# Performance work log

Hardware: AMD Instinct MI355X
Metric: run time of the kernel (lower is better)

The kernel has to match this reference:

```python
import jax, jax.numpy as jnp
import numpy as np

EMBED_DIM = 1024
NUM_HEADS = 16
HEAD_DIM = EMBED_DIM // NUM_HEADS


def setup_inputs() -> dict:
    key = jax.random.key(0)
    ks = jax.random.split(key, 5)
    s = 0.02
    return {
        "x": jax.random.normal(ks[0], (2, 2048, EMBED_DIM), dtype=jnp.float32),
        "w_qkv": jax.random.normal(ks[1], (EMBED_DIM, 3 * EMBED_DIM), dtype=jnp.float32) * s,
        "b_qkv": jnp.zeros((3 * EMBED_DIM,), dtype=jnp.float32),
        "w_out": jax.random.normal(ks[2], (EMBED_DIM, EMBED_DIM), dtype=jnp.float32) * s,
        "b_out": jnp.zeros((EMBED_DIM,), dtype=jnp.float32),
    }


def reference(x, w_qkv, b_qkv, w_out, b_out):
    B, T, C = x.shape
    qkv = x @ w_qkv + b_qkv                       # [B,T,3C]
    q, k, v = jnp.split(qkv, 3, axis=-1)
    # [B,T,C] -> [B,H,T,Dh]
    def heads(t):
        return t.reshape(B, T, NUM_HEADS, HEAD_DIM).transpose(0, 2, 1, 3)
    q, k, v = heads(q), heads(k), heads(v)
    scale = 1.0 / np.sqrt(HEAD_DIM).astype(np.float32)
    scores = jnp.einsum("bhqd,bhkd->bhqk", q, k) * scale  # [B,H,T,T]
    causal = jnp.tril(jnp.ones((T, T), dtype=bool))
    scores = jnp.where(causal[None, None], scores, -jnp.inf)
    attn = jax.nn.softmax(scores, axis=-1)
    out = jnp.einsum("bhqk,bhkd->bhqd", attn, v)  # [B,H,T,Dh]
    out = out.transpose(0, 2, 1, 3).reshape(B, T, C)
    return out @ w_out + b_out
```

## Files before the change

kernel.cpp:

```cpp
#include <hip/hip_runtime.h>

typedef unsigned short u16;
typedef unsigned int u32;
typedef __attribute__((ext_vector_type(2))) unsigned int u32x2;
typedef __attribute__((ext_vector_type(8))) short bf16x8;
typedef __attribute__((ext_vector_type(4))) float f32x4;
typedef __attribute__((ext_vector_type(16))) float f32x16;

#define TOK   4096
#define EMB   1024
#define NQKV  3072
#define TSEQ  2048
#define NH    16

__device__ __forceinline__ u16 f2b(float f) {
  union { float f; unsigned u; } v; v.f = f;
  unsigned r = v.u + 0x7FFFu + ((v.u >> 16) & 1u);
  return (u16)(r >> 16);
}

__device__ __forceinline__ u16 f2b_hu(float f) {
  return (u16)((__float_as_uint(f) + 0x8000u) >> 16);
}

__device__ __forceinline__ u32 pack_rn(float a, float b) {
  u32 ua = __float_as_uint(a) + 0x8000u;
  u32 ub = __float_as_uint(b) + 0x8000u;
  return __builtin_amdgcn_perm(ub, ua, 0x07060302u);
}

__device__ __forceinline__ f32x16 zero16() {
  f32x16 z;
#pragma unroll
  for (int i = 0; i < 16; i++) z[i] = 0.f;
  return z;
}

__device__ __forceinline__ void gload16(const void* g, void* l) {
  __builtin_amdgcn_global_load_lds((const __attribute__((address_space(1))) void*)g,
                                   (__attribute__((address_space(3))) void*)l, 16, 0, 0);
}


__global__ __launch_bounds__(256) void prep_kernel(const float* __restrict__ x,
                                                   u16* __restrict__ x_bf,
                                                   const float* __restrict__ w_qkv,
                                                   u16* __restrict__ wqkvT,
                                                   const float* __restrict__ w_out,
                                                   u16* __restrict__ woutT) {
  __shared__ u16 sm[64][65];
  int bid = blockIdx.x, tid = threadIdx.x;
  if (bid < 4096) {
    int i = bid * 256 + tid;
    float4 v = ((const float4*)x)[i];
    union { u16 us[4]; uint2 u2; } o;
    o.us[0] = f2b(v.x); o.us[1] = f2b(v.y); o.us[2] = f2b(v.z); o.us[3] = f2b(v.w);
    ((uint2*)x_bf)[i] = o.u2;
    return;
  }
  const float* src; u16* dst; int R, C, bx, by;
  if (bid < 4096 + 768) {
    int t = bid - 4096; bx = t % 48; by = t / 48;
    src = w_qkv; dst = wqkvT; R = EMB; C = NQKV;
  } else {
    int t = bid - 4096 - 768; bx = t & 15; by = t >> 4;
    src = w_out; dst = woutT; R = EMB; C = EMB;
  }
  int c0 = bx * 64, r0 = by * 64;
#pragma unroll
  for (int i = 0; i < 16; i++) {
    int idx = tid + i * 256;
    int r = idx >> 6, c = idx & 63;
    sm[r][c] = f2b(src[(size_t)(r0 + r) * C + c0 + c]);
  }
  __syncthreads();
  int cc2 = tid >> 2, rr0 = (tid & 3) * 16;
  union { u16 us[16]; uint4 v4[2]; } o;
#pragma unroll
  for (int j = 0; j < 16; j++) o.us[j] = sm[rr0 + j][cc2];
  *(uint4*)&dst[(size_t)(c0 + cc2) * R + r0 + rr0]     = o.v4[0];
  *(uint4*)&dst[(size_t)(c0 + cc2) * R + r0 + rr0 + 8] = o.v4[1];
}


template <int MODE, int TN>
__global__ __launch_bounds__(256) void gemm_bt(const u16* __restrict__ A,
                                               const u16* __restrict__ Bt,
                                               const float* __restrict__ bias,
                                               u16* __restrict__ qb, u16* __restrict__ kb,
                                               u16* __restrict__ vb, float* __restrict__ outp,
                                               int K, int N) {
  constexpr int CT = TN / 32;
  constexpr int RB = TN / 32;
  __shared__ u16 As[2][128][64];
  __shared__ u16 Bs[2][TN][64];
  int tid = threadIdx.x;
  int m0 = blockIdx.y * 128, n0 = blockIdx.x * TN;
  int lane = tid & 63, wid = tid >> 6;
  int wm = (wid >> 1) * 64;
  int wn = (wid & 1) * (TN / 2);
  int l15 = lane & 15, quad = lane >> 4;
  int srow = lane >> 3;
  int scol = (((lane & 7) ^ srow) * 8);

  f32x4 acc[4][CT];
#pragma unroll
  for (int i = 0; i < 4; i++)
#pragma unroll
    for (int j = 0; j < CT; j++) acc[i][j] = (f32x4){0.f, 0.f, 0.f, 0.f};

  const u16* Ag = A + (size_t)(m0 + wid * 32 + srow) * K + scol;
  const u16* Bg = Bt + (size_t)(n0 + wid * (TN / 4) + srow) * K + scol;

#pragma unroll
  for (int i = 0; i < 4; i++)
    gload16(Ag + (size_t)(i * 8) * K, &As[0][wid * 32 + i * 8][0]);
#pragma unroll
  for (int i = 0; i < RB; i++)
    gload16(Bg + (size_t)(i * 8) * K, &Bs[0][wid * (TN / 4) + i * 8][0]);
  __syncthreads();

  int cur = 0;
  for (int k0 = 0; k0 < K; k0 += 64) {
    if (k0 + 64 < K) {
      int kn = k0 + 64;
#pragma unroll
      for (int i = 0; i < 4; i++)
        gload16(Ag + (size_t)(i * 8) * K + kn, &As[cur ^ 1][wid * 32 + i * 8][0]);
#pragma unroll
      for (int i = 0; i < RB; i++)
        gload16(Bg + (size_t)(i * 8) * K + kn, &Bs[cur ^ 1][wid * (TN / 4) + i * 8][0]);
    }

#pragma unroll
    for (int ks = 0; ks < 2; ks++) {
      bf16x8 af[4], bfr[CT];
#pragma unroll
      for (int rt = 0; rt < 4; rt++)
        af[rt] = *(const bf16x8*)&As[cur][wm + rt * 16 + l15][((ks * 4 + quad) ^ (l15 & 7)) * 8];
#pragma unroll
      for (int ct = 0; ct < CT; ct++)
        bfr[ct] = *(const bf16x8*)&Bs[cur][wn + ct * 16 + l15][((ks * 4 + quad) ^ (l15 & 7)) * 8];
#pragma unroll
      for (int rt = 0; rt < 4; rt++)
#pragma unroll
        for (int ct = 0; ct < CT; ct++)
          acc[rt][ct] = __builtin_amdgcn_mfma_f32_16x16x32_bf16(bfr[ct], af[rt], acc[rt][ct], 0, 0, 0);
    }
    __syncthreads();
    cur ^= 1;
  }

#pragma unroll
  for (int rt = 0; rt < 4; rt++) {
#pragma unroll
    for (int ct = 0; ct < CT; ct++) {
      int m = m0 + wm + rt * 16 + l15;
      int nb = n0 + wn + ct * 16 + quad * 4;
      float4 b4 = *(const float4*)&bias[nb];
      float v0 = acc[rt][ct][0] + b4.x, v1 = acc[rt][ct][1] + b4.y;
      float v2 = acc[rt][ct][2] + b4.z, v3 = acc[rt][ct][3] + b4.w;
      if (MODE == 0) {
        int sel = nb >> 10;
        int c = nb & 1023;
        int h = c >> 6, d0 = c & 63;
        int b = m >> 11, t = m & 2047;
        if (sel == 2) {
          size_t vbase = ((((size_t)b * NH + h) * 64 + d0) * TSEQ) + t;
          vb[vbase]            = f2b_hu(v0);
          vb[vbase + TSEQ]     = f2b_hu(v1);
          vb[vbase + 2 * TSEQ] = f2b_hu(v2);
          vb[vbase + 3 * TSEQ] = f2b_hu(v3);
        } else {
          u16* dst = sel ? kb : qb;
          union { u32 u[2]; uint2 u2; } o;
          o.u[0] = pack_rn(v0, v1);
          o.u[1] = pack_rn(v2, v3);
          *(uint2*)&dst[((((size_t)b * NH + h) * TSEQ + t) << 6) + d0] = o.u2;
        }
      } else {
        float4 o = {v0, v1, v2, v3};
        *(float4*)&outp[(size_t)m * N + nb] = o;
      }
    }
  }
}


__global__ __launch_bounds__(256, 4) void attn_kernel(const u16* __restrict__ Qb,
                                                      const u16* __restrict__ Kb,
                                                      const u16* __restrict__ Vtb,
                                                      u16* __restrict__ O) {
  __shared__ u16 Ks[64][68];
  __shared__ u16 Vt[64][68];
  __shared__ float Cmb[2][16][64][2];
  __shared__ float Lmb[2][32];

  const float SCL = 0.18033688f;
  const float MOFF = 16.0f;

  int phys = blockIdx.x;
  int xcd = phys & 7;
  int cuL = (phys >> 3) & 31;
  int slot = phys >> 8;
  int bh = xcd * 4 + slot;
  int qt = (slot & 1) ? (31 - cuL) : cuL;

  int tid = threadIdx.x, lane = tid & 63, w = tid >> 6;
  int sub = w & 1, par = w >> 1;
  int l31 = lane & 31, h = lane >> 5;
  const size_t hoff = (size_t)bh * TSEQ * 64;

  int qw = qt * 64 + sub * 32;
  int qg = qw + l31;

  bf16x8 qf[4];
  {
    const u16* qp = Qb + hoff + (size_t)qg * 64 + h * 8;
#pragma unroll
    for (int s = 0; s < 4; s++) qf[s] = *(const bf16x8*)(qp + s * 16);
  }

  f32x16 acc[2];
  acc[0] = zero16(); acc[1] = zero16();
  float l_i = 0.f;

  int r = tid >> 2, cb = (tid & 3) * 16;
  bf16x8 kr0, kr1, vr0, vr1;
  {
    const u16* kg = Kb + hoff + (size_t)r * 64 + cb;
    const u16* vg = Vtb + hoff + (size_t)r * TSEQ + cb;
    kr0 = *(const bf16x8*)kg;       kr1 = *(const bf16x8*)(kg + 8);
    vr0 = *(const bf16x8*)vg;       vr1 = *(const bf16x8*)(vg + 8);
  }

  for (int kt = 0; kt <= qt; kt++) {
    __syncthreads();
    *(bf16x8*)&Ks[r][cb]     = kr0;
    *(bf16x8*)&Ks[r][cb + 8] = kr1;
    *(bf16x8*)&Vt[r][cb]     = vr0;
    *(bf16x8*)&Vt[r][cb + 8] = vr1;
    __syncthreads();
    if (kt < qt) {
      const u16* kg = Kb + hoff + (size_t)((kt + 1) * 64 + r) * 64 + cb;
      const u16* vg = Vtb + hoff + (size_t)r * TSEQ + (kt + 1) * 64 + cb;
      kr0 = *(const bf16x8*)kg;     kr1 = *(const bf16x8*)(kg + 8);
      vr0 = *(const bf16x8*)vg;     vr1 = *(const bf16x8*)(vg + 8);
    }

    int kbt = kt * 64 + par * 32;
    if (kbt <= qw + 31) {
      f32x16 sacc = zero16();
      __builtin_amdgcn_s_setprio(1);
#pragma unroll
      for (int s = 0; s < 4; s++) {
        bf16x8 kf = *(const bf16x8*)&Ks[par * 32 + l31][s * 16 + h * 8];
        sacc = __builtin_amdgcn_mfma_f32_32x32x16_bf16(kf, qf[s], sacc, 0, 0, 0);
      }
      __builtin_amdgcn_s_setprio(0);

      if (kbt + 31 > qw) {
#pragma unroll
        for (int rr = 0; rr < 16; rr++) {
          int key = kbt + (rr & 3) + 8 * (rr >> 2) + 4 * h;
          if (key > qg) sacc[rr] = -1e30f;
        }
      }

#pragma unroll
      for (int rr = 0; rr < 16; rr++) {
        float p = exp2f(__builtin_fmaf(sacc[rr], SCL, -MOFF));
        sacc[rr] = p;
        l_i += p;
      }

#pragma unroll
      for (int s2 = 0; s2 < 2; s2++) {
        u32 u0, u1, u2, u3;
        asm("v_cvt_pk_bf16_f32 %0, %1, %2" : "=v"(u0) : "v"(sacc[8 * s2 + 0]), "v"(sacc[8 * s2 + 1]));
        asm("v_cvt_pk_bf16_f32 %0, %1, %2" : "=v"(u1) : "v"(sacc[8 * s2 + 2]), "v"(sacc[8 * s2 + 3]));
        asm("v_cvt_pk_bf16_f32 %0, %1, %2" : "=v"(u2) : "v"(sacc[8 * s2 + 4]), "v"(sacc[8 * s2 + 5]));
        asm("v_cvt_pk_bf16_f32 %0, %1, %2" : "=v"(u3) : "v"(sacc[8 * s2 + 6]), "v"(sacc[8 * s2 + 7]));
        u32x2 r02 = __builtin_amdgcn_permlane32_swap(u0, u2, false, false);
        u32x2 r13 = __builtin_amdgcn_permlane32_swap(u1, u3, false, false);
        union { u32 d[4]; bf16x8 v; } pf;
        pf.d[0] = r02[0];
        pf.d[1] = r13[0];
        pf.d[2] = r02[1];
        pf.d[3] = r13[1];
        __builtin_amdgcn_s_setprio(1);
#pragma unroll
        for (int dt = 0; dt < 2; dt++) {
          bf16x8 vf = *(const bf16x8*)&Vt[dt * 32 + l31][par * 32 + s2 * 16 + h * 8];
          acc[dt] = __builtin_amdgcn_mfma_f32_32x32x16_bf16(vf, pf.v, acc[dt], 0, 0, 0);
        }
        __builtin_amdgcn_s_setprio(0);
      }
    }
  }

  l_i += __shfl_xor(l_i, 32);

  __syncthreads();
  if (par == 1) {
#pragma unroll
    for (int dt = 0; dt < 2; dt++)
#pragma unroll
      for (int pr = 0; pr < 8; pr++) {
        Cmb[sub][dt * 8 + pr][lane][0] = acc[dt][2 * pr];
        Cmb[sub][dt * 8 + pr][lane][1] = acc[dt][2 * pr + 1];
      }
    if (h == 0) Lmb[sub][l31] = l_i;
  }
  __syncthreads();
  if (par == 0) {
#pragma unroll
    for (int dt = 0; dt < 2; dt++)
#pragma unroll
      for (int pr = 0; pr < 8; pr++) {
        acc[dt][2 * pr]     += Cmb[sub][dt * 8 + pr][lane][0];
        acc[dt][2 * pr + 1] += Cmb[sub][dt * 8 + pr][lane][1];
      }
    float lt = l_i + Lmb[sub][l31];
    float inv = 1.0f / lt;

    int b = bh >> 4, head = bh & 15;
    size_t rowbase = ((size_t)b * TSEQ + qg) * 1024 + head * 64;
#pragma unroll
    for (int dt = 0; dt < 2; dt++)
#pragma unroll
      for (int G = 0; G < 4; G++) {
        union { u32 u[2]; uint2 u2; } o;
        o.u[0] = pack_rn(acc[dt][4 * G + 0] * inv, acc[dt][4 * G + 1] * inv);
        o.u[1] = pack_rn(acc[dt][4 * G + 2] * inv, acc[dt][4 * G + 3] * inv);
        *(uint2*)&O[rowbase + dt * 32 + G * 8 + 4 * h] = o.u2;
      }
  }
}


extern "C" void kernel_launch(void* const* d_in, const int* in_sizes, int n_in,
                              void* d_out, int out_size, void* d_ws, size_t ws_size,
                              hipStream_t stream) {
  (void)in_sizes; (void)n_in; (void)out_size; (void)ws_size;
  const float* x     = (const float*)d_in[0];
  const float* w_qkv = (const float*)d_in[1];
  const float* b_qkv = (const float*)d_in[2];
  const float* w_out = (const float*)d_in[3];
  const float* b_out = (const float*)d_in[4];
  float* out = (float*)d_out;

  char* p = (char*)d_ws;
  u16* x_bf  = (u16*)p; p += (size_t)TOK * EMB * 2;
  u16* wqkvT = (u16*)p; p += (size_t)NQKV * EMB * 2;
  u16* woutT = (u16*)p; p += (size_t)EMB * EMB * 2;
  u16* Qb    = (u16*)p; p += (size_t)32 * TSEQ * 64 * 2;
  u16* Kb    = (u16*)p; p += (size_t)32 * TSEQ * 64 * 2;
  u16* Vtb   = (u16*)p; p += (size_t)32 * TSEQ * 64 * 2;
  u16* attn_o = (u16*)p;

  prep_kernel<<<dim3(4096 + 768 + 256), 256, 0, stream>>>(x, x_bf, w_qkv, wqkvT, w_out, woutT);
  gemm_bt<0, 128><<<dim3(NQKV / 128, TOK / 128), 256, 0, stream>>>(x_bf, wqkvT, b_qkv,
                                                                   Qb, Kb, Vtb, nullptr, EMB, NQKV);
  attn_kernel<<<dim3(1024), 256, 0, stream>>>(Qb, Kb, Vtb, attn_o);
  gemm_bt<1, 64><<<dim3(EMB / 64, TOK / 128), 256, 0, stream>>>(attn_o, woutT, b_out,
                                                                nullptr, nullptr, nullptr, out, EMB, EMB);
}
```

Measured before the change: 181.4 us.

## Add dedicated 256x192-tile QKV GEMM with 512 threads and interleaved prefetch

Replaces the generic 128x128 gemm_bt for the QKV projection with a specialized kernel using 256x192 tiles, 8 waves, and launch_bounds(512,1). Global-to-LDS prefetch of the next K step is split into phases interleaved with MFMA groups, with s_barrier and setprio around compute. The larger tile raises arithmetic intensity per LDS byte, and the grid becomes 16x16=256 blocks, roughly one per CU. The cost is heavier register and LDS use, and a single wave of blocks leaves no slack for load imbalance.

```diff
diff --git a/kernel.cpp b/kernel.cpp
--- a/kernel.cpp
+++ b/kernel.cpp
@@ -80,6 +80,119 @@
   for (int j = 0; j < 16; j++) o.us[j] = sm[rr0 + j][cc2];
   *(uint4*)&dst[(size_t)(c0 + cc2) * R + r0 + rr0]     = o.v4[0];
   *(uint4*)&dst[(size_t)(c0 + cc2) * R + r0 + rr0 + 8] = o.v4[1];
+}
+
+
+__global__ __launch_bounds__(512, 1) void gemm_qkv(const u16* __restrict__ A,
+                                                   const u16* __restrict__ Bt,
+                                                   const float* __restrict__ bias,
+                                                   u16* __restrict__ qb, u16* __restrict__ kb,
+                                                   u16* __restrict__ vb) {
+  constexpr int K = EMB;
+  constexpr int NSTEP = K / 64;
+  __shared__ u16 As[2][256][64];
+  __shared__ u16 Bs[2][192][64];
+  int tid = threadIdx.x;
+  int m0 = blockIdx.y * 256, n0 = blockIdx.x * 192;
+  int lane = tid & 63, wid = tid >> 6;
+  int wm = (wid >> 2) * 128;
+  int wn = (wid & 3) * 48;
+  int l15 = lane & 15, quad = lane >> 4;
+  int srow = lane >> 3;
+  int scol = ((lane & 7) ^ srow) * 8;
+
+  f32x4 acc[8][3];
+#pragma unroll
+  for (int i = 0; i < 8; i++)
+#pragma unroll
+    for (int j = 0; j < 3; j++) acc[i][j] = (f32x4){0.f, 0.f, 0.f, 0.f};
+
+  const u16* Ag = A + (size_t)(m0 + wid * 32 + srow) * K + scol;
+  const u16* Bg = Bt + (size_t)(n0 + wid * 24 + srow) * K + scol;
+
+#pragma unroll
+  for (int i = 0; i < 4; i++)
+    gload16(Ag + (size_t)(i * 8) * K, &As[0][wid * 32 + i * 8][0]);
+#pragma unroll
+  for (int i = 0; i < 3; i++)
+    gload16(Bg + (size_t)(i * 8) * K, &Bs[0][wid * 24 + i * 8][0]);
+  __syncthreads();
+
+  for (int t = 0; t < NSTEP; t++) {
+    int cur = t & 1;
+    int kn = (t + 1) * 64;
+    bool pf = (t + 1 < NSTEP);
+    bf16x8 bfr[3];
+#pragma unroll
+    for (int ks = 0; ks < 2; ks++) {
+#pragma unroll
+      for (int rh = 0; rh < 2; rh++) {
+        const int ph = ks * 2 + rh;
+        if (pf) {
+          if (ph == 0) {
+            gload16(Ag + (size_t)0 * K + kn,  &As[cur ^ 1][wid * 32 + 0][0]);
+            gload16(Ag + (size_t)8 * K + kn,  &As[cur ^ 1][wid * 32 + 8][0]);
+          } else if (ph == 1) {
+            gload16(Ag + (size_t)16 * K + kn, &As[cur ^ 1][wid * 32 + 16][0]);
+            gload16(Ag + (size_t)24 * K + kn, &As[cur ^ 1][wid * 32 + 24][0]);
+          } else if (ph == 2) {
+            gload16(Bg + (size_t)0 * K + kn,  &Bs[cur ^ 1][wid * 24 + 0][0]);
+            gload16(Bg + (size_t)8 * K + kn,  &Bs[cur ^ 1][wid * 24 + 8][0]);
+          } else {
+            gload16(Bg + (size_t)16 * K + kn, &Bs[cur ^ 1][wid * 24 + 16][0]);
+          }
+        }
+        if (rh == 0) {
+#pragma unroll
+          for (int ct = 0; ct < 3; ct++)
+            bfr[ct] = *(const bf16x8*)&Bs[cur][wn + ct * 16 + l15][((ks * 4 + quad) ^ (l15 & 7)) * 8];
+        }
+        bf16x8 af[4];
+#pragma unroll
+        for (int i = 0; i < 4; i++)
+          af[i] = *(const bf16x8*)&As[cur][wm + (rh * 4 + i) * 16 + l15][((ks * 4 + quad) ^ (l15 & 7)) * 8];
+        __builtin_amdgcn_s_barrier();
+        __builtin_amdgcn_s_setprio(1);
+#pragma unroll
+        for (int i = 0; i < 4; i++)
+#pragma unroll
+          for (int ct = 0; ct < 3; ct++)
+            acc[rh * 4 + i][ct] = __builtin_amdgcn_mfma_f32_16x16x32_bf16(bfr[ct], af[i], acc[rh * 4 + i][ct], 0, 0, 0);
+        __builtin_amdgcn_s_setprio(0);
+        __builtin_amdgcn_s_barrier();
+      }
+    }
+    __syncthreads();
+  }
+
+#pragma unroll
+  for (int rt = 0; rt < 8; rt++) {
+#pragma unroll
+    for (int ct = 0; ct < 3; ct++) {
+      int m = m0 + wm + rt * 16 + l15;
+      int nb = n0 + wn + ct * 16 + quad * 4;
+      float4 b4 = *(const float4*)&bias[nb];
+      float v0 = acc[rt][ct][0] + b4.x, v1 = acc[rt][ct][1] + b4.y;
+      float v2 = acc[rt][ct][2] + b4.z, v3 = acc[rt][ct][3] + b4.w;
+      int sel = nb >> 10;
+      int c = nb & 1023;
+      int h = c >> 6, d0 = c & 63;
+      int b = m >> 11, tt = m & 2047;
+      if (sel == 2) {
+        size_t vbase = ((((size_t)b * NH + h) * 64 + d0) * TSEQ) + tt;
+        vb[vbase]            = f2b_hu(v0);
+        vb[vbase + TSEQ]     = f2b_hu(v1);
+        vb[vbase + 2 * TSEQ] = f2b_hu(v2);
+        vb[vbase + 3 * TSEQ] = f2b_hu(v3);
+      } else {
+        u16* dst = sel ? kb : qb;
+        union { u32 u[2]; uint2 u2; } o;
+        o.u[0] = pack_rn(v0, v1);
+        o.u[1] = pack_rn(v2, v3);
+        *(uint2*)&dst[((((size_t)b * NH + h) * TSEQ + tt) << 6) + d0] = o.u2;
+      }
+    }
+  }
 }
 
 
@@ -360,8 +473,7 @@
   u16* attn_o = (u16*)p;
 
   prep_kernel<<<dim3(4096 + 768 + 256), 256, 0, stream>>>(x, x_bf, w_qkv, wqkvT, w_out, woutT);
-  gemm_bt<0, 128><<<dim3(NQKV / 128, TOK / 128), 256, 0, stream>>>(x_bf, wqkvT, b_qkv,
-                                                                   Qb, Kb, Vtb, nullptr, EMB, NQKV);
+  gemm_qkv<<<dim3(NQKV / 192, TOK / 256), 512, 0, stream>>>(x_bf, wqkvT, b_qkv, Qb, Kb, Vtb);
   attn_kernel<<<dim3(1024), 256, 0, stream>>>(Qb, Kb, Vtb, attn_o);
   gemm_bt<1, 64><<<dim3(EMB / 64, TOK / 128), 256, 0, stream>>>(attn_o, woutT, b_out,
                                                                 nullptr, nullptr, nullptr, out, EMB, EMB);
```

Result: slower. 189.9 us (+4.7%).
